# Kernel tuning notes

Hardware: AMD Instinct MI355X
Metric: run time of the kernel (lower is better)

## Reference

```python
import jax, jax.numpy as jnp
import numpy as np

COV_EMB = 32
N_HEAD = 2
FACTOR_TCL = 2   # TemporalConvolutionalLayer factor (default 2)
FACTOR_MLP = 1   # MLP factor passed from MultiAttention init
EPS = 1e-5


def _conv1d_causal(x, w, b):
    # x: [N, C, T], w: [O, C, 3]; torch pads 2 both sides then slices [..., :-2],
    # equivalent to left-pad 2 only -> output length T.
    y = jax.lax.conv_general_dilated(x, w, window_strides=(1,), padding=[(2, 0)],
                                     dimension_numbers=('NCH', 'OIH', 'NCH'))
    return y + b[None, :, None]


def _tcl(x, w_conv, b_conv, w_proj, b_proj):
    # TemporalConvolutionalLayer: x [..., T, C] -> [..., T, C]
    shp = x.shape
    T, C = shp[-2], shp[-1]
    x2 = x.reshape(-1, T, C).transpose(0, 2, 1)              # [N, C, T]
    h = jax.nn.gelu(_conv1d_causal(x2, w_conv, b_conv), approximate=False)
    h = h.transpose(0, 2, 1)                                  # [N, T, 2C]
    out = h @ w_proj.T + b_proj                               # [N, T, C]
    return out.reshape(*shp[:-1], C)


def _layernorm(x, w):
    mu = jnp.mean(x, axis=-1, keepdims=True)
    var = jnp.var(x, axis=-1, keepdims=True)
    return (x - mu) * jax.lax.rsqrt(var + EPS) * w


def setup_inputs() -> dict:
    key = jax.random.key(0)
    ks = jax.random.split(key, 20)
    C = COV_EMB
    C2 = FACTOR_TCL * C
    s = 0.02
    inp = {
        'causal_decoder': jax.random.normal(ks[0], (8, 4, 1024, C), jnp.float32),
        'past_kv': jax.random.normal(ks[1], (8, 1024, C), jnp.float32),
    }
    def tcl_params(i):
        return (jax.random.normal(ks[i], (C2, C, 3), jnp.float32) * s,
                jnp.zeros((C2,), jnp.float32),
                jax.random.normal(ks[i + 1], (C, C2), jnp.float32) * s,
                jnp.zeros((C,), jnp.float32))
    inp['wq_conv'], inp['bq_conv'], inp['wq_proj'], inp['bq_proj'] = tcl_params(2)
    inp['wk_conv'], inp['bk_conv'], inp['wk_proj'], inp['bk_proj'] = tcl_params(4)
    inp['wv_conv'], inp['bv_conv'], inp['wv_proj'], inp['bv_proj'] = tcl_params(6)
    inp['w_cproj'] = jax.random.normal(ks[8], (C, C), jnp.float32) * s   # bias=False
    inp['ln_w'] = jnp.ones((C,), jnp.float32)                            # bias=False
    inp['w_fc'] = jax.random.normal(ks[9], (FACTOR_MLP * C, C), jnp.float32) * s   # bias=False
    inp['w_mlp_proj'] = jax.random.normal(ks[10], (C, FACTOR_MLP * C), jnp.float32) * s
    return inp


def reference(causal_decoder, past_kv,
              wq_conv, bq_conv, wq_proj, bq_proj,
              wk_conv, bk_conv, wk_proj, bk_proj,
              wv_conv, bv_conv, wv_proj, bv_proj,
              w_cproj, ln_w, w_fc, w_mlp_proj):
    B, F, T, C = causal_decoder.shape
    nh, hd = N_HEAD, C // N_HEAD

    q = _tcl(causal_decoder, wq_conv, bq_conv, wq_proj, bq_proj)   # [B,F,T,C]
    k = _tcl(past_kv, wk_conv, bk_conv, wk_proj, bk_proj)          # [B,S,C]
    v = _tcl(past_kv, wv_conv, bv_conv, wv_proj, bv_proj)          # [B,S,C]

    S = k.shape[1]
    q = q.reshape(B, F, T, nh, hd).transpose(0, 1, 3, 2, 4)        # [B,F,h,T,d]
    k = k.reshape(B, S, nh, hd).transpose(0, 2, 1, 3)              # [B,h,S,d]
    v = v.reshape(B, S, nh, hd).transpose(0, 2, 1, 3)              # [B,h,S,d]

    scale = 1.0 / jnp.sqrt(jnp.asarray(hd, q.dtype))
    scores = jnp.einsum('bfhtd,bhsd->bfhts', q, k) * scale          # [B,F,h,T,S]
    attn = jax.nn.softmax(scores, axis=-1)
    y = jnp.einsum('bfhts,bhsd->bfhtd', attn, v)                    # [B,F,h,T,d]
    y = y.transpose(0, 1, 3, 2, 4).reshape(B, F, T, C)

    out = causal_decoder + y @ w_cproj.T                            # resid_dropout = id (p=0)
    h = _layernorm(out, ln_w)
    mlp = jax.nn.gelu(h @ w_fc.T, approximate=False) @ w_mlp_proj.T
    out = out + mlp
    return out
```

## Files before the change

### kernel.cpp

```cpp
#include <hip/hip_runtime.h>
#include <hip/hip_bf16.h>

#define T_LEN 1024

typedef __attribute__((ext_vector_type(8))) short short8;
typedef __attribute__((ext_vector_type(4))) short short4v;
typedef __attribute__((ext_vector_type(4))) float float4v;
typedef __attribute__((ext_vector_type(2))) unsigned uint2v;
typedef __attribute__((ext_vector_type(4))) unsigned uint4v;

__device__ __forceinline__ float gelu_exact(float x) {
    return 0.5f * x * (1.0f + erff(x * 0.70710678118654752440f));
}
__device__ __forceinline__ unsigned short f2bf(float f) {
    unsigned u = __float_as_uint(f);
    u += 0x7fffu + ((u >> 16) & 1u);
    return (unsigned short)(u >> 16);
}
__device__ __forceinline__ unsigned pk2bf(float a, float b) {
    __hip_bfloat162 h = __float22bfloat162_rn(make_float2(a, b));
    unsigned u;
    __builtin_memcpy(&u, &h, 4);
    return u;
}

__device__ __forceinline__ short8 xpose_p(float4v t0, float4v t1) {
    unsigned u0 = pk2bf(t0.x, t0.y);
    unsigned u1 = pk2bf(t0.z, t0.w);
    unsigned u2 = pk2bf(t1.x, t1.y);
    unsigned u3 = pk2bf(t1.z, t1.w);
    uint2v r0 = __builtin_amdgcn_permlane32_swap(u0, u2, false, false);
    uint2v r1 = __builtin_amdgcn_permlane32_swap(u1, u3, false, false);
    uint2v r2 = __builtin_amdgcn_permlane16_swap(r0.x, r0.y, false, false);
    uint2v r3 = __builtin_amdgcn_permlane16_swap(r1.x, r1.y, false, false);
    uint4v p = { r2.x, r3.x, r2.y, r3.y };
    short8 f;
    __builtin_memcpy(&f, &p, 16);
    return f;
}

__global__ __launch_bounds__(256) void kv_tcl(
    const float* __restrict__ pkv,
    const float* __restrict__ wkc, const float* __restrict__ bkc,
    const float* __restrict__ wkp, const float* __restrict__ bkp,
    const float* __restrict__ wvc, const float* __restrict__ bvc,
    const float* __restrict__ wvp, const float* __restrict__ bvp,
    unsigned short* __restrict__ kbf, unsigned short* __restrict__ vtbf)
{
    __shared__ __align__(16) unsigned short Abuf[32 * 96];
    __shared__ __align__(16) unsigned short WbT[64 * 96];
    __shared__ __align__(16) unsigned short Hb[32 * 72];
    __shared__ __align__(16) unsigned short WpB[32 * 72];

    const int tid = threadIdx.x;
    const int gb = blockIdx.x;

    const float *wc, *bc, *wp, *bp;
    unsigned short* outb;
    int n, mode;
    if (gb < 256) { n = gb >> 5;         wc = wkc; bc = bkc; wp = wkp; bp = bkp; outb = kbf;  mode = 0; }
    else          { n = (gb - 256) >> 5; wc = wvc; bc = bvc; wp = wvp; bp = bvp; outb = vtbf; mode = 1; }
    const int t0 = (gb & 31) * 32;

#pragma unroll
    for (int it = 0; it < 3; ++it) {
        int s = (tid + it * 256) >> 3;
        int sub = tid & 7;
        int t = s / 3, tap = s - t * 3;
        int tau = t0 + t - 2 + tap;
        float4 xv = make_float4(0.f, 0.f, 0.f, 0.f);
        if (tau >= 0) xv = *(const float4*)&pkv[((size_t)n * T_LEN + tau) * 32 + sub * 4];
        short4v pk = { (short)f2bf(xv.x), (short)f2bf(xv.y),
                       (short)f2bf(xv.z), (short)f2bf(xv.w) };
        *(short4v*)&Abuf[t * 96 + tap * 32 + sub * 4] = pk;
    }
#pragma unroll
    for (int it = 0; it < 6; ++it) {
        int i4 = tid + it * 256;
        int idx = i4 * 4;
        int o = idx / 96, r = idx - o * 96;
        float4 w4 = *(const float4*)&wc[idx];
        float we[4] = { w4.x, w4.y, w4.z, w4.w };
#pragma unroll
        for (int e = 0; e < 4; ++e) {
            int re = r + e, c = re / 3, tap = re - c * 3;
            WbT[o * 96 + tap * 32 + c] = f2bf(we[e]);
        }
    }
#pragma unroll
    for (int it = 0; it < 2; ++it) {
        int i4 = tid + it * 256;
        int idx = i4 * 4;
        int c = idx >> 6, o = idx & 63;
        float4 w4 = *(const float4*)&wp[idx];
        short4v pk = { (short)f2bf(w4.x), (short)f2bf(w4.y),
                       (short)f2bf(w4.z), (short)f2bf(w4.w) };
        *(short4v*)&WpB[c * 72 + o] = pk;
    }

    const int w = tid >> 6;
    const int ln = tid & 63;
    const int sn = ln & 15;
    const int quad = ln >> 4;

    const float bcv = bc[w * 16 + sn];
    const int tmw = w & 1, cnw = w >> 1;
    const float bpv = bp[cnw * 16 + sn];

    __syncthreads();

    short8 b0 = *(const short8*)&WbT[(w * 16 + sn) * 96 + 0  + quad * 8];
    short8 b1 = *(const short8*)&WbT[(w * 16 + sn) * 96 + 32 + quad * 8];
    short8 b2 = *(const short8*)&WbT[(w * 16 + sn) * 96 + 64 + quad * 8];
    float4v zero = { 0.f, 0.f, 0.f, 0.f };
    float4v acc[2] = { zero, zero };
#pragma unroll
    for (int tm = 0; tm < 2; ++tm) {
        const unsigned short* ar = &Abuf[(tm * 16 + sn) * 96 + quad * 8];
        short8 a0 = *(const short8*)(ar + 0);
        short8 a1 = *(const short8*)(ar + 32);
        short8 a2 = *(const short8*)(ar + 64);
        acc[tm] = __builtin_amdgcn_mfma_f32_16x16x32_bf16(a0, b0, acc[tm], 0, 0, 0);
        acc[tm] = __builtin_amdgcn_mfma_f32_16x16x32_bf16(a1, b1, acc[tm], 0, 0, 0);
        acc[tm] = __builtin_amdgcn_mfma_f32_16x16x32_bf16(a2, b2, acc[tm], 0, 0, 0);
    }
#pragma unroll
    for (int tm = 0; tm < 2; ++tm) {
        float ge[4];
        ge[0] = gelu_exact(acc[tm].x + bcv);
        ge[1] = gelu_exact(acc[tm].y + bcv);
        ge[2] = gelu_exact(acc[tm].z + bcv);
        ge[3] = gelu_exact(acc[tm].w + bcv);
#pragma unroll
        for (int i = 0; i < 4; ++i)
            Hb[(tm * 16 + quad * 4 + i) * 72 + w * 16 + sn] = f2bf(ge[i]);
    }

    __syncthreads();

    const unsigned short* hr = &Hb[(tmw * 16 + sn) * 72 + quad * 8];
    short8 pa0 = *(const short8*)(hr + 0);
    short8 pa1 = *(const short8*)(hr + 32);
    short8 pb0 = *(const short8*)&WpB[(cnw * 16 + sn) * 72 + quad * 8];
    short8 pb1 = *(const short8*)&WpB[(cnw * 16 + sn) * 72 + 32 + quad * 8];
    float4v pacc = zero;
    pacc = __builtin_amdgcn_mfma_f32_16x16x32_bf16(pa0, pb0, pacc, 0, 0, 0);
    pacc = __builtin_amdgcn_mfma_f32_16x16x32_bf16(pa1, pb1, pacc, 0, 0, 0);

    float v[4] = { pacc.x + bpv, pacc.y + bpv, pacc.z + bpv, pacc.w + bpv };
#pragma unroll
    for (int i = 0; i < 4; ++i) {
        int t = tmw * 16 + quad * 4 + i;
        int c = cnw * 16 + sn;
        if (mode == 0) {
            outb[((size_t)n * T_LEN + t0 + t) * 32 + c] = f2bf(v[i]);
        } else {
            outb[((size_t)(n * 2 + cnw) * 16 + sn) * T_LEN + t0 + t] = f2bf(v[i]);
        }
    }
}

__global__ __launch_bounds__(512) void fused_qae(
    const float* __restrict__ cd,
    const float* __restrict__ wqc, const float* __restrict__ bqc,
    const float* __restrict__ wqp, const float* __restrict__ bqp,
    const unsigned short* __restrict__ kbf,
    const unsigned short* __restrict__ vtbf,
    const float* __restrict__ wcp, const float* __restrict__ lnw,
    const float* __restrict__ wfc, const float* __restrict__ wmp,
    float* __restrict__ out)
{
    __shared__ __align__(16) char smem[43520];
    unsigned short* Abuf = (unsigned short*)(smem);
    unsigned short* WbT  = (unsigned short*)(smem + 12288);
    unsigned short* Hb   = (unsigned short*)(smem + 24576);
    unsigned short* WpB  = (unsigned short*)(smem + 33792);
    unsigned short* qs   = (unsigned short*)(smem + 38400);

    const int tid = threadIdx.x;
    const int bf = blockIdx.x >> 4;
    const int tt = blockIdx.x & 15;
    const int t0 = tt * 64;
    const int b = bf >> 2;
    const float SC = 0.36067376022224085f;

#pragma unroll
    for (int it = 0; it < 3; ++it) {
        int idx = tid + it * 512;
        int s = idx >> 3;
        int sub = idx & 7;
        int t = s / 3, tap = s - t * 3;
        int tau = t0 + t - 2 + tap;
        float4 xv = make_float4(0.f, 0.f, 0.f, 0.f);
        if (tau >= 0) xv = *(const float4*)&cd[((size_t)bf * T_LEN + tau) * 32 + sub * 4];
        short4v pk = { (short)f2bf(xv.x), (short)f2bf(xv.y),
                       (short)f2bf(xv.z), (short)f2bf(xv.w) };
        *(short4v*)&Abuf[t * 96 + tap * 32 + sub * 4] = pk;
    }
#pragma unroll
    for (int it = 0; it < 3; ++it) {
        int i4 = tid + it * 512;
        int idx = i4 * 4;
        int o = idx / 96, r = idx - o * 96;
        float4 w4 = *(const float4*)&wqc[idx];
        float we[4] = { w4.x, w4.y, w4.z, w4.w };
#pragma unroll
        for (int e = 0; e < 4; ++e) {
            int re = r + e, c = re / 3, tap = re - c * 3;
            WbT[o * 96 + tap * 32 + c] = f2bf(we[e]);
        }
    }
    {
        int idx = tid * 4;
        int c = idx >> 6, o = idx & 63;
        float4 w4 = *(const float4*)&wqp[idx];
        short4v pk = { (short)f2bf(w4.x), (short)f2bf(w4.y),
                       (short)f2bf(w4.z), (short)f2bf(w4.w) };
        *(short4v*)&WpB[c * 72 + o] = pk;
    }

    const int w = tid >> 6;
    const int ln = tid & 63;
    const int sn = ln & 15;
    const int quad = ln >> 4;
    const float4v zero = { 0.f, 0.f, 0.f, 0.f };

    __syncthreads();

    {
        const int tm = w & 3;
        const int on0 = w >> 2, on1 = on0 + 2;
        const unsigned short* ar = &Abuf[(tm * 16 + sn) * 96 + quad * 8];
        short8 a0 = *(const short8*)(ar + 0);
        short8 a1 = *(const short8*)(ar + 32);
        short8 a2 = *(const short8*)(ar + 64);
        const unsigned short* br0 = &WbT[(on0 * 16 + sn) * 96 + quad * 8];
        const unsigned short* br1 = &WbT[(on1 * 16 + sn) * 96 + quad * 8];
        float4v c0 = zero, c1 = zero;
        c0 = __builtin_amdgcn_mfma_f32_16x16x32_bf16(a0, *(const short8*)(br0 + 0),  c0, 0, 0, 0);
        c0 = __builtin_amdgcn_mfma_f32_16x16x32_bf16(a1, *(const short8*)(br0 + 32), c0, 0, 0, 0);
        c0 = __builtin_amdgcn_mfma_f32_16x16x32_bf16(a2, *(const short8*)(br0 + 64), c0, 0, 0, 0);
        c1 = __builtin_amdgcn_mfma_f32_16x16x32_bf16(a0, *(const short8*)(br1 + 0),  c1, 0, 0, 0);
        c1 = __builtin_amdgcn_mfma_f32_16x16x32_bf16(a1, *(const short8*)(br1 + 32), c1, 0, 0, 0);
        c1 = __builtin_amdgcn_mfma_f32_16x16x32_bf16(a2, *(const short8*)(br1 + 64), c1, 0, 0, 0);
        const float bc0 = bqc[on0 * 16 + sn], bc1 = bqc[on1 * 16 + sn];
        float g0[4] = { gelu_exact(c0.x + bc0), gelu_exact(c0.y + bc0),
                        gelu_exact(c0.z + bc0), gelu_exact(c0.w + bc0) };
        float g1[4] = { gelu_exact(c1.x + bc1), gelu_exact(c1.y + bc1),
                        gelu_exact(c1.z + bc1), gelu_exact(c1.w + bc1) };
#pragma unroll
        for (int i = 0; i < 4; ++i) {
            Hb[(tm * 16 + quad * 4 + i) * 72 + on0 * 16 + sn] = f2bf(g0[i]);
            Hb[(tm * 16 + quad * 4 + i) * 72 + on1 * 16 + sn] = f2bf(g1[i]);
        }
    }
    __syncthreads();

    {
        const int tm = w & 3, cn = w >> 2;
        const unsigned short* hr = &Hb[(tm * 16 + sn) * 72 + quad * 8];
        short8 pa0 = *(const short8*)(hr + 0);
        short8 pa1 = *(const short8*)(hr + 32);
        const unsigned short* wr_ = &WpB[(cn * 16 + sn) * 72 + quad * 8];
        short8 pb0 = *(const short8*)(wr_ + 0);
        short8 pb1 = *(const short8*)(wr_ + 32);
        float4v pacc = zero;
        pacc = __builtin_amdgcn_mfma_f32_16x16x32_bf16(pa0, pb0, pacc, 0, 0, 0);
        pacc = __builtin_amdgcn_mfma_f32_16x16x32_bf16(pa1, pb1, pacc, 0, 0, 0);
        const float bpv = bqp[cn * 16 + sn];
        float v[4] = { (pacc.x + bpv) * SC, (pacc.y + bpv) * SC,
                       (pacc.z + bpv) * SC, (pacc.w + bpv) * SC };
#pragma unroll
        for (int i = 0; i < 4; ++i)
            qs[(tm * 16 + quad * 4 + i) * 40 + cn * 16 + sn] = f2bf(v[i]);
    }

    {
        float* swc = (float*)(smem + 0);
        float* swf = (float*)(smem + 4608);
        float* swm = (float*)(smem + 9216);
        float* sln = (float*)(smem + 13824);
        for (int i = tid; i < 1024; i += 512) {
            int r = i >> 5, cc = i & 31;
            swc[r * 36 + cc] = wcp[i];
            swf[r * 36 + cc] = wfc[i];
            swm[r * 36 + cc] = wmp[i];
        }
        if (tid < 32) sln[tid] = lnw[tid];
    }
    __syncthreads();

    const int h = w & 1, rt = w >> 1;
    short8 aq = {0, 0, 0, 0, 0, 0, 0, 0};
    if (quad < 2)
        aq = *(const short8*)&qs[(rt * 16 + sn) * 40 + h * 16 + quad * 8];

    const unsigned short* kb = kbf + (size_t)b * T_LEN * 32 + h * 16 + quad * 8;
    const unsigned short* vb = vtbf + ((size_t)(b * 2 + h) * 16 + sn) * T_LEN + quad * 8;

    const short8 ones = { 16256, 16256, 16256, 16256,
                          16256, 16256, 16256, 16256 };
    float4v yacc = zero;
    float4v lacc = zero;

#pragma unroll 2
    for (int s0 = 0; s0 < 1024; s0 += 64) {
        short8 ka0 = {0,0,0,0,0,0,0,0}, ka1 = ka0, kc0 = ka0, kc1 = ka0;
        if (quad < 2) {
            ka0 = *(const short8*)(kb + (size_t)(s0 + sn) * 32);
            ka1 = *(const short8*)(kb + (size_t)(s0 + 16 + sn) * 32);
            kc0 = *(const short8*)(kb + (size_t)(s0 + 32 + sn) * 32);
            kc1 = *(const short8*)(kb + (size_t)(s0 + 48 + sn) * 32);
        }
        short8 bvA = *(const short8*)(vb + s0);
        short8 bvB = *(const short8*)(vb + s0 + 32);

        float4v cA0 = __builtin_amdgcn_mfma_f32_16x16x32_bf16(ka0, aq, zero, 0, 0, 0);
        float4v cA1 = __builtin_amdgcn_mfma_f32_16x16x32_bf16(ka1, aq, zero, 0, 0, 0);
        float4v cB0 = __builtin_amdgcn_mfma_f32_16x16x32_bf16(kc0, aq, zero, 0, 0, 0);
        float4v cB1 = __builtin_amdgcn_mfma_f32_16x16x32_bf16(kc1, aq, zero, 0, 0, 0);

        float4v eA0, eA1, eB0, eB1;
        eA0.x = exp2f(cA0.x); eA0.y = exp2f(cA0.y); eA0.z = exp2f(cA0.z); eA0.w = exp2f(cA0.w);
        eA1.x = exp2f(cA1.x); eA1.y = exp2f(cA1.y); eA1.z = exp2f(cA1.z); eA1.w = exp2f(cA1.w);
        eB0.x = exp2f(cB0.x); eB0.y = exp2f(cB0.y); eB0.z = exp2f(cB0.z); eB0.w = exp2f(cB0.w);
        eB1.x = exp2f(cB1.x); eB1.y = exp2f(cB1.y); eB1.z = exp2f(cB1.z); eB1.w = exp2f(cB1.w);

        short8 apA = xpose_p(eA0, eA1);
        short8 apB = xpose_p(eB0, eB1);

        yacc = __builtin_amdgcn_mfma_f32_16x16x32_bf16(bvA, apA, yacc, 0, 0, 0);
        yacc = __builtin_amdgcn_mfma_f32_16x16x32_bf16(bvB, apB, yacc, 0, 0, 0);
        lacc = __builtin_amdgcn_mfma_f32_16x16x32_bf16(ones, apA, lacc, 0, 0, 0);
        lacc = __builtin_amdgcn_mfma_f32_16x16x32_bf16(ones, apB, lacc, 0, 0, 0);
    }

    float* sy = (float*)(smem + 24576);
    {
        const float linv = 1.0f / lacc.x;
        float4v yn = { yacc.x * linv, yacc.y * linv,
                       yacc.z * linv, yacc.w * linv };
        *(float4v*)&sy[(rt * 16 + sn) * 32 + h * 16 + quad * 4] = yn;
    }
    __syncthreads();

    float* swc = (float*)(smem + 0);
    float* swf = (float*)(smem + 4608);
    float* swm = (float*)(smem + 9216);
    float* sln = (float*)(smem + 13824);
    float* shn = (float*)(smem + 13952);
    float* sgv = (float*)(smem + 16256);

    const int rl = tid >> 5, c = tid & 31;
    const float lnwc = sln[c];
#pragma unroll 1
    for (int p = 0; p < 4; ++p) {
        int r = p * 16 + rl;
        size_t row = (size_t)bf * T_LEN + t0 + r;
        float x1 = cd[row * 32 + c];
#pragma unroll
        for (int j4 = 0; j4 < 8; ++j4) {
            float4 yv = *(const float4*)&sy[r * 32 + j4 * 4];
            const float* wv = &swc[c * 36 + j4 * 4];
            x1 += wv[0] * yv.x + wv[1] * yv.y + wv[2] * yv.z + wv[3] * yv.w;
        }
        float s1 = x1, s2 = x1 * x1;
#pragma unroll
        for (int off = 16; off; off >>= 1) {
            s1 += __shfl_xor(s1, off);
            s2 += __shfl_xor(s2, off);
        }
        float mu = s1 * (1.0f / 32.0f);
        float var = s2 * (1.0f / 32.0f) - mu * mu;
        float hn = (x1 - mu) * rsqrtf(var + 1e-5f) * lnwc;
        shn[rl * 36 + c] = hn;
        float ga = 0.f;
#pragma unroll
        for (int j4 = 0; j4 < 8; ++j4) {
            float4 hv = *(const float4*)&shn[rl * 36 + j4 * 4];
            const float* wv = &swf[c * 36 + j4 * 4];
            ga += wv[0] * hv.x + wv[1] * hv.y + wv[2] * hv.z + wv[3] * hv.w;
        }
        float gv = gelu_exact(ga);
        sgv[rl * 36 + c] = gv;
        float oa = x1;
#pragma unroll
        for (int j4 = 0; j4 < 8; ++j4) {
            float4 gvv = *(const float4*)&sgv[rl * 36 + j4 * 4];
            const float* wv = &swm[c * 36 + j4 * 4];
            oa += wv[0] * gvv.x + wv[1] * gvv.y + wv[2] * gvv.z + wv[3] * gvv.w;
        }
        out[row * 32 + c] = oa;
    }
}

extern "C" void kernel_launch(void* const* d_in, const int* in_sizes, int n_in,
                              void* d_out, int out_size, void* d_ws, size_t ws_size,
                              hipStream_t stream) {
    const float* cd  = (const float*)d_in[0];
    const float* pkv = (const float*)d_in[1];
    const float* wqc = (const float*)d_in[2];
    const float* bqc = (const float*)d_in[3];
    const float* wqp = (const float*)d_in[4];
    const float* bqp = (const float*)d_in[5];
    const float* wkc = (const float*)d_in[6];
    const float* bkc = (const float*)d_in[7];
    const float* wkp = (const float*)d_in[8];
    const float* bkp = (const float*)d_in[9];
    const float* wvc = (const float*)d_in[10];
    const float* bvc = (const float*)d_in[11];
    const float* wvp = (const float*)d_in[12];
    const float* bvp = (const float*)d_in[13];
    const float* wcp = (const float*)d_in[14];
    const float* lnw = (const float*)d_in[15];
    const float* wfc = (const float*)d_in[16];
    const float* wmp = (const float*)d_in[17];

    unsigned short* kbf  = (unsigned short*)d_ws;
    unsigned short* vtbf = kbf + (size_t)8 * 1024 * 32;

    kv_tcl<<<512, 256, 0, stream>>>(pkv, wkc, bkc, wkp, bkp,
                                    wvc, bvc, wvp, bvp, kbf, vtbf);
    fused_qae<<<512, 512, 0, stream>>>(cd, wqc, bqc, wqp, bqp, kbf, vtbf,
                                       wcp, lnw, wfc, wmp, (float*)d_out);
}
```

Before: 131.7 us.

## Split attention key range across two wave groups with 1024-thread blocks

Doubles the fused kernel's block to 1024 threads. The attention loop over keys is split into two halves, each handled by a separate set of 8 waves, and the partial numerators and denominators are combined in shared memory before the output projection and MLP. Weight staging is overlapped with the Q projection by assigning it to the upper waves, and exp2f is replaced by a raw v_exp_f32 instruction. This shortens the serial per-wave softmax loop and raises parallelism, at the cost of more shared memory, extra reduction work, and possibly lower occupancy per CU.

Measured after the change: 135.4 us. +2.8%, slower.

```diff
diff --git a/kernel.cpp b/kernel.cpp
--- a/kernel.cpp
+++ b/kernel.cpp
@@ -22,6 +22,11 @@
     unsigned u;
     __builtin_memcpy(&u, &h, 4);
     return u;
+}
+__device__ __forceinline__ float fexp2(float x) {
+    float r;
+    asm("v_exp_f32 %0, %1" : "=v"(r) : "v"(x));
+    return r;
 }
 
 __device__ __forceinline__ short8 xpose_p(float4v t0, float4v t1) {
@@ -160,7 +165,7 @@
     }
 }
 
-__global__ __launch_bounds__(512) void fused_qae(
+__global__ __launch_bounds__(1024, 8) void fused_qae(
     const float* __restrict__ cd,
     const float* __restrict__ wqc, const float* __restrict__ bqc,
     const float* __restrict__ wqp, const float* __restrict__ bqp,
@@ -170,7 +175,7 @@
     const float* __restrict__ wfc, const float* __restrict__ wmp,
     float* __restrict__ out)
 {
-    __shared__ __align__(16) char smem[43520];
+    __shared__ __align__(16) char smem[52736];
     unsigned short* Abuf = (unsigned short*)(smem);
     unsigned short* WbT  = (unsigned short*)(smem + 12288);
     unsigned short* Hb   = (unsigned short*)(smem + 24576);
@@ -185,32 +190,36 @@
     const float SC = 0.36067376022224085f;
 
 #pragma unroll
-    for (int it = 0; it < 3; ++it) {
-        int idx = tid + it * 512;
-        int s = idx >> 3;
-        int sub = idx & 7;
-        int t = s / 3, tap = s - t * 3;
-        int tau = t0 + t - 2 + tap;
-        float4 xv = make_float4(0.f, 0.f, 0.f, 0.f);
-        if (tau >= 0) xv = *(const float4*)&cd[((size_t)bf * T_LEN + tau) * 32 + sub * 4];
-        short4v pk = { (short)f2bf(xv.x), (short)f2bf(xv.y),
-                       (short)f2bf(xv.z), (short)f2bf(xv.w) };
-        *(short4v*)&Abuf[t * 96 + tap * 32 + sub * 4] = pk;
-    }
-#pragma unroll
-    for (int it = 0; it < 3; ++it) {
-        int i4 = tid + it * 512;
-        int idx = i4 * 4;
-        int o = idx / 96, r = idx - o * 96;
-        float4 w4 = *(const float4*)&wqc[idx];
-        float we[4] = { w4.x, w4.y, w4.z, w4.w };
-#pragma unroll
-        for (int e = 0; e < 4; ++e) {
-            int re = r + e, c = re / 3, tap = re - c * 3;
-            WbT[o * 96 + tap * 32 + c] = f2bf(we[e]);
-        }
-    }
-    {
+    for (int it = 0; it < 2; ++it) {
+        int idx = tid + it * 1024;
+        if (idx < 1536) {
+            int s = idx >> 3;
+            int sub = idx & 7;
+            int t = s / 3, tap = s - t * 3;
+            int tau = t0 + t - 2 + tap;
+            float4 xv = make_float4(0.f, 0.f, 0.f, 0.f);
+            if (tau >= 0) xv = *(const float4*)&cd[((size_t)bf * T_LEN + tau) * 32 + sub * 4];
+            short4v pk = { (short)f2bf(xv.x), (short)f2bf(xv.y),
+                           (short)f2bf(xv.z), (short)f2bf(xv.w) };
+            *(short4v*)&Abuf[t * 96 + tap * 32 + sub * 4] = pk;
+        }
+    }
+#pragma unroll
+    for (int it = 0; it < 2; ++it) {
+        int i4 = tid + it * 1024;
+        if (i4 < 1536) {
+            int idx = i4 * 4;
+            int o = idx / 96, r = idx - o * 96;
+            float4 w4 = *(const float4*)&wqc[idx];
+            float we[4] = { w4.x, w4.y, w4.z, w4.w };
+#pragma unroll
+            for (int e = 0; e < 4; ++e) {
+                int re = r + e, c = re / 3, tap = re - c * 3;
+                WbT[o * 96 + tap * 32 + c] = f2bf(we[e]);
+            }
+        }
+    }
+    if (tid < 512) {
         int idx = tid * 4;
         int c = idx >> 6, o = idx & 63;
         float4 w4 = *(const float4*)&wqp[idx];
@@ -229,34 +238,26 @@
 
     {
         const int tm = w & 3;
-        const int on0 = w >> 2, on1 = on0 + 2;
+        const int on = w >> 2;
         const unsigned short* ar = &Abuf[(tm * 16 + sn) * 96 + quad * 8];
         short8 a0 = *(const short8*)(ar + 0);
         short8 a1 = *(const short8*)(ar + 32);
         short8 a2 = *(const short8*)(ar + 64);
-        const unsigned short* br0 = &WbT[(on0 * 16 + sn) * 96 + quad * 8];
-        const unsigned short* br1 = &WbT[(on1 * 16 + sn) * 96 + quad * 8];
-        float4v c0 = zero, c1 = zero;
-        c0 = __builtin_amdgcn_mfma_f32_16x16x32_bf16(a0, *(const short8*)(br0 + 0),  c0, 0, 0, 0);
-        c0 = __builtin_amdgcn_mfma_f32_16x16x32_bf16(a1, *(const short8*)(br0 + 32), c0, 0, 0, 0);
-        c0 = __builtin_amdgcn_mfma_f32_16x16x32_bf16(a2, *(const short8*)(br0 + 64), c0, 0, 0, 0);
-        c1 = __builtin_amdgcn_mfma_f32_16x16x32_bf16(a0, *(const short8*)(br1 + 0),  c1, 0, 0, 0);
-        c1 = __builtin_amdgcn_mfma_f32_16x16x32_bf16(a1, *(const short8*)(br1 + 32), c1, 0, 0, 0);
-        c1 = __builtin_amdgcn_mfma_f32_16x16x32_bf16(a2, *(const short8*)(br1 + 64), c1, 0, 0, 0);
-        const float bc0 = bqc[on0 * 16 + sn], bc1 = bqc[on1 * 16 + sn];
+        const unsigned short* br = &WbT[(on * 16 + sn) * 96 + quad * 8];
+        float4v c0 = zero;
+        c0 = __builtin_amdgcn_mfma_f32_16x16x32_bf16(a0, *(const short8*)(br + 0),  c0, 0, 0, 0);
+        c0 = __builtin_amdgcn_mfma_f32_16x16x32_bf16(a1, *(const short8*)(br + 32), c0, 0, 0, 0);
+        c0 = __builtin_amdgcn_mfma_f32_16x16x32_bf16(a2, *(const short8*)(br + 64), c0, 0, 0, 0);
+        const float bc0 = bqc[on * 16 + sn];
         float g0[4] = { gelu_exact(c0.x + bc0), gelu_exact(c0.y + bc0),
                         gelu_exact(c0.z + bc0), gelu_exact(c0.w + bc0) };
-        float g1[4] = { gelu_exact(c1.x + bc1), gelu_exact(c1.y + bc1),
-                        gelu_exact(c1.z + bc1), gelu_exact(c1.w + bc1) };
-#pragma unroll
-        for (int i = 0; i < 4; ++i) {
-            Hb[(tm * 16 + quad * 4 + i) * 72 + on0 * 16 + sn] = f2bf(g0[i]);
-            Hb[(tm * 16 + quad * 4 + i) * 72 + on1 * 16 + sn] = f2bf(g1[i]);
-        }
-    }
-    __syncthreads();
-
-    {
+#pragma unroll
+        for (int i = 0; i < 4; ++i)
+            Hb[(tm * 16 + quad * 4 + i) * 72 + on * 16 + sn] = f2bf(g0[i]);
+    }
+    __syncthreads();
+
+    if (w < 8) {
         const int tm = w & 3, cn = w >> 2;
         const unsigned short* hr = &Hb[(tm * 16 + sn) * 72 + quad * 8];
         short8 pa0 = *(const short8*)(hr + 0);
@@ -273,24 +274,23 @@
 #pragma unroll
         for (int i = 0; i < 4; ++i)
             qs[(tm * 16 + quad * 4 + i) * 40 + cn * 16 + sn] = f2bf(v[i]);
-    }
-
-    {
+    } else {
         float* swc = (float*)(smem + 0);
         float* swf = (float*)(smem + 4608);
         float* swm = (float*)(smem + 9216);
         float* sln = (float*)(smem + 13824);
-        for (int i = tid; i < 1024; i += 512) {
+        int t2 = tid - 512;
+        for (int i = t2; i < 1024; i += 512) {
             int r = i >> 5, cc = i & 31;
             swc[r * 36 + cc] = wcp[i];
             swf[r * 36 + cc] = wfc[i];
             swm[r * 36 + cc] = wmp[i];
         }
-        if (tid < 32) sln[tid] = lnw[tid];
-    }
-    __syncthreads();
-
-    const int h = w & 1, rt = w >> 1;
+        if (t2 < 32) sln[t2] = lnw[t2];
+    }
+    __syncthreads();
+
+    const int h = w & 1, rt = (w >> 1) & 3, sh = w >> 3;
     short8 aq = {0, 0, 0, 0, 0, 0, 0, 0};
     if (quad < 2)
         aq = *(const short8*)&qs[(rt * 16 + sn) * 40 + h * 16 + quad * 8];
@@ -303,8 +303,9 @@
     float4v yacc = zero;
     float4v lacc = zero;
 
+    int s0 = sh << 9;
 #pragma unroll 2
-    for (int s0 = 0; s0 < 1024; s0 += 64) {
+    for (int ii = 0; ii < 8; ++ii, s0 += 64) {
         short8 ka0 = {0,0,0,0,0,0,0,0}, ka1 = ka0, kc0 = ka0, kc1 = ka0;
         if (quad < 2) {
             ka0 = *(const short8*)(kb + (size_t)(s0 + sn) * 32);
@@ -321,10 +322,10 @@
         float4v cB1 = __builtin_amdgcn_mfma_f32_16x16x32_bf16(kc1, aq, zero, 0, 0, 0);
 
         float4v eA0, eA1, eB0, eB1;
-        eA0.x = exp2f(cA0.x); eA0.y = exp2f(cA0.y); eA0.z = exp2f(cA0.z); eA0.w = exp2f(cA0.w);
-        eA1.x = exp2f(cA1.x); eA1.y = exp2f(cA1.y); eA1.z = exp2f(cA1.z); eA1.w = exp2f(cA1.w);
-        eB0.x = exp2f(cB0.x); eB0.y = exp2f(cB0.y); eB0.z = exp2f(cB0.z); eB0.w = exp2f(cB0.w);
-        eB1.x = exp2f(cB1.x); eB1.y = exp2f(cB1.y); eB1.z = exp2f(cB1.z); eB1.w = exp2f(cB1.w);
+        eA0.x = fexp2(cA0.x); eA0.y = fexp2(cA0.y); eA0.z = fexp2(cA0.z); eA0.w = fexp2(cA0.w);
+        eA1.x = fexp2(cA1.x); eA1.y = fexp2(cA1.y); eA1.z = fexp2(cA1.z); eA1.w = fexp2(cA1.w);
+        eB0.x = fexp2(cB0.x); eB0.y = fexp2(cB0.y); eB0.z = fexp2(cB0.z); eB0.w = fexp2(cB0.w);
+        eB1.x = fexp2(cB1.x); eB1.y = fexp2(cB1.y); eB1.z = fexp2(cB1.z); eB1.w = fexp2(cB1.w);
 
         short8 apA = xpose_p(eA0, eA1);
         short8 apB = xpose_p(eB0, eB1);
@@ -335,12 +336,11 @@
         lacc = __builtin_amdgcn_mfma_f32_16x16x32_bf16(ones, apB, lacc, 0, 0, 0);
     }
 
-    float* sy = (float*)(smem + 24576);
     {
-        const float linv = 1.0f / lacc.x;
-        float4v yn = { yacc.x * linv, yacc.y * linv,
-                       yacc.z * linv, yacc.w * linv };
-        *(float4v*)&sy[(rt * 16 + sn) * 32 + h * 16 + quad * 4] = yn;
+        float* syp = (float*)(smem + (sh ? 43520 : 24576));
+        *(float4v*)&syp[(rt * 16 + sn) * 32 + h * 16 + quad * 4] = yacc;
+        float* lbuf = (float*)(smem + 51712);
+        if (quad == 0) lbuf[(sh * 2 + h) * 64 + rt * 16 + sn] = lacc.x;
     }
     __syncthreads();
 
@@ -349,18 +349,28 @@
     float* swm = (float*)(smem + 9216);
     float* sln = (float*)(smem + 13824);
     float* shn = (float*)(smem + 13952);
-    float* sgv = (float*)(smem + 16256);
+    float* sgv = (float*)(smem + 18560);
+    float* sy0 = (float*)(smem + 24576);
+    float* sy1 = (float*)(smem + 43520);
+    float* lbuf = (float*)(smem + 51712);
 
     const int rl = tid >> 5, c = tid & 31;
     const float lnwc = sln[c];
 #pragma unroll 1
-    for (int p = 0; p < 4; ++p) {
-        int r = p * 16 + rl;
+    for (int p = 0; p < 2; ++p) {
+        int r = p * 32 + rl;
         size_t row = (size_t)bf * T_LEN + t0 + r;
+        const float li0 = 1.0f / (lbuf[r] + lbuf[128 + r]);
+        const float li1 = 1.0f / (lbuf[64 + r] + lbuf[192 + r]);
         float x1 = cd[row * 32 + c];
 #pragma unroll
         for (int j4 = 0; j4 < 8; ++j4) {
-            float4 yv = *(const float4*)&sy[r * 32 + j4 * 4];
+            const float sc = (j4 < 4) ? li0 : li1;
+            int yi = r * 32 + j4 * 4;
+            float4 y0 = *(const float4*)&sy0[yi];
+            float4 y1 = *(const float4*)&sy1[yi];
+            float4 yv = make_float4((y0.x + y1.x) * sc, (y0.y + y1.y) * sc,
+                                    (y0.z + y1.z) * sc, (y0.w + y1.w) * sc);
             const float* wv = &swc[c * 36 + j4 * 4];
             x1 += wv[0] * yv.x + wv[1] * yv.y + wv[2] * yv.z + wv[3] * yv.w;
         }
@@ -421,6 +431,6 @@
 
     kv_tcl<<<512, 256, 0, stream>>>(pkv, wkc, bkc, wkp, bkp,
                                     wvc, bvc, wvp, bvp, kbf, vtbf);
-    fused_qae<<<512, 512, 0, stream>>>(cd, wqc, bqc, wqp, bqp, kbf, vtbf,
-                                       wcp, lnw, wfc, wmp, (float*)d_out);
-}
+    fused_qae<<<512, 1024, 0, stream>>>(cd, wqc, bqc, wqp, bqp, kbf, vtbf,
+                                        wcp, lnw, wfc, wmp, (float*)d_out);
+}
```
